# Performance work log

Hardware: AMD Instinct MI355X
Metric: run time of the kernel (lower is better)

The kernel has to match this reference:

```python
import jax, jax.numpy as jnp
import numpy as np

B = 4096
N_DENSE = 13
N_SPARSE = 26
FEAT_PER_SPARSE = 1000
FIELD_NUM = N_DENSE + N_SPARSE          # 39
FEATURE_NUM = N_DENSE + N_SPARSE * FEAT_PER_SPARSE  # 26013
K = 16


def setup_inputs() -> dict:
    key = jax.random.key(0)
    k1, k2, k3, k4 = jax.random.split(key, 4)
    dense_inputs = jax.random.normal(k1, (B, N_DENSE), dtype=jnp.float32)
    sparse_inputs = jax.random.randint(k2, (B, N_SPARSE), 0, FEAT_PER_SPARSE, dtype=jnp.int32)
    w0 = jnp.zeros((1,), dtype=jnp.float32)
    w = jax.random.normal(k3, (FEATURE_NUM, 1), dtype=jnp.float32) * 0.05
    v = jax.random.normal(k4, (FEATURE_NUM, FIELD_NUM, K), dtype=jnp.float32) * 0.05
    return {"dense_inputs": dense_inputs, "sparse_inputs": sparse_inputs,
            "w0": w0, "w": w, "v": v}


def reference(dense_inputs, sparse_inputs, w0, w, v):
    # Feature-index layout matches tf.concat([dense cols, one_hot(sparse_0), ...]):
    # rows [0, N_DENSE) of w/v belong to dense fields, then FEAT_PER_SPARSE rows per sparse field.
    offsets = N_DENSE + FEAT_PER_SPARSE * jnp.arange(N_SPARSE, dtype=sparse_inputs.dtype)
    idx = sparse_inputs + offsets[None, :]               # [B, n_sparse] global feature ids

    # First order: w0 + onehot_concat @ w  ==  w0 + dense part + gathered sparse rows
    first_order = (w0
                   + dense_inputs @ w[:N_DENSE]                       # [B, 1]
                   + jnp.sum(w[idx, 0], axis=1, keepdims=True))       # [B, 1]

    # field_f = tensordot(onehot_concat, v) -> [B, field_num, k]
    field_f = (jnp.einsum('bd,dfk->bfk', dense_inputs, v[:N_DENSE])
               + jnp.sum(v[idx], axis=1))                             # [B, F, K]

    # sum_{i<j} <f_i, f_j> = 0.5 * (||sum_i f_i||^2 - sum_i ||f_i||^2)  (FM identity)
    s = jnp.sum(field_f, axis=1)                                      # [B, K]
    second_order = 0.5 * (jnp.sum(s * s, axis=-1)
                          - jnp.sum(field_f * field_f, axis=(1, 2)))  # [B]
    return first_order + second_order[:, None]
```

## Files before the change

### kernel.cpp

```cpp
#include <hip/hip_runtime.h>

#define NDENSE 13
#define NSPARSE 26
#define ROW_F4 156
#define BATCH 4096
#define RPB 64
#define CHUNKS (BATCH / RPB)
#define SL_PER_XCD 5

__global__ __launch_bounds__(256) void ffm_slice3(
    const float*  __restrict__ dense,
    const int*    __restrict__ sparse,
    const float4* __restrict__ v4,
    float4*       __restrict__ ff)
{
    const int xcd   = blockIdx.x & 7;
    const int rest  = blockIdx.x >> 3;
    const int slice = xcd * SL_PER_XCD + (rest >> 6);
    const int chunk = rest & (CHUNKS - 1);

    __shared__ int    vrow_s[RPB * NSPARSE];
    __shared__ float  dsh   [RPB * NDENSE];
    __shared__ float4 vsh   [NDENSE * 4];

    if (slice >= 39) return;

    const int t = threadIdx.x;
    const int row0 = chunk * RPB;
    for (int i = t; i < RPB * NSPARSE; i += 256) {
        const int r = i / NSPARSE, j = i % NSPARSE;
        vrow_s[i] = sparse[(row0 + r) * NSPARSE + j] + NDENSE + 1000 * j;
    }
    for (int i = t; i < RPB * NDENSE; i += 256)
        dsh[i] = dense[row0 * NDENSE + i];
    if (t < NDENSE * 4)
        vsh[t] = v4[(t >> 2) * ROW_F4 + slice * 4 + (t & 3)];
    __syncthreads();

    const int lane = t & 63;
    const int wv   = t >> 6;
    const int rl   = (wv << 4) + (lane >> 2);
    const int c    = lane & 3;
    const int fb   = slice * 4 + c;

    float4 acc = make_float4(0.f, 0.f, 0.f, 0.f);
#pragma unroll
    for (int d = 0; d < NDENSE; ++d) {
        const float  wg = dsh[rl * NDENSE + d];
        const float4 vv = vsh[d * 4 + c];
        acc.x += wg * vv.x; acc.y += wg * vv.y;
        acc.z += wg * vv.z; acc.w += wg * vv.w;
    }

    float4 g[NSPARSE];
#pragma unroll
    for (int j = 0; j < NSPARSE; ++j)
        g[j] = v4[(unsigned)vrow_s[rl * NSPARSE + j] * ROW_F4 + fb];
#pragma unroll
    for (int j = 0; j < NSPARSE; ++j) {
        acc.x += g[j].x; acc.y += g[j].y; acc.z += g[j].z; acc.w += g[j].w;
    }

    ff[(unsigned)(row0 + rl) * ROW_F4 + fb] = acc;
}

__global__ __launch_bounds__(256) void ffm_final(
    const float*  __restrict__ dense,
    const int*    __restrict__ sparse,
    const float*  __restrict__ w0,
    const float*  __restrict__ w,
    const float4* __restrict__ ff,
    float*        __restrict__ out)
{
    const int wave = threadIdx.x >> 6;
    const int lane = threadIdx.x & 63;
    const int b = blockIdx.x * 4 + wave;

    float4 s = make_float4(0.f, 0.f, 0.f, 0.f);
    float  sq = 0.f;
#pragma unroll
    for (int p = 0; p < 3; ++p) {
        const int e4 = lane + 64 * p;
        if (e4 < ROW_F4) {
            const float4 acc = ff[(unsigned)b * ROW_F4 + e4];
            s.x += acc.x; s.y += acc.y; s.z += acc.z; s.w += acc.w;
            sq  += acc.x*acc.x + acc.y*acc.y + acc.z*acc.z + acc.w*acc.w;
        }
    }
#pragma unroll
    for (int m = 4; m <= 32; m <<= 1) {
        s.x += __shfl_xor(s.x, m); s.y += __shfl_xor(s.y, m);
        s.z += __shfl_xor(s.z, m); s.w += __shfl_xor(s.w, m);
    }
    float s2 = s.x*s.x + s.y*s.y + s.z*s.z + s.w*s.w;
    s2 += __shfl_xor(s2, 1);
    s2 += __shfl_xor(s2, 2);
#pragma unroll
    for (int m = 1; m <= 32; m <<= 1) sq += __shfl_xor(sq, m);

    float fo = 0.f;
    if (lane < NSPARSE) fo = w[sparse[b * NSPARSE + lane] + NDENSE + 1000 * lane];
    if (lane < NDENSE)  fo += dense[b * NDENSE + lane] * w[lane];
#pragma unroll
    for (int m = 1; m <= 32; m <<= 1) fo += __shfl_xor(fo, m);

    if (lane == 0) out[b] = w0[0] + fo + 0.5f * (s2 - sq);
}

__global__ __launch_bounds__(256) void ffm_fused(
    const float* __restrict__ dense, const int* __restrict__ sparse,
    const float* __restrict__ w0, const float* __restrict__ w,
    const float4* __restrict__ v4, float* __restrict__ out)
{
    const int wave = threadIdx.x >> 6;
    const int lane = threadIdx.x & 63;
    const int b = blockIdx.x * 4 + wave;

    float dv[NDENSE];
#pragma unroll
    for (int d = 0; d < NDENSE; ++d) dv[d] = dense[b * NDENSE + d];
    int myidx = 0;
    if (lane < NSPARSE) myidx = sparse[b * NSPARSE + lane] + NDENSE + 1000 * lane;

    float4 s = make_float4(0.f, 0.f, 0.f, 0.f);
    float  sq = 0.f;
#pragma unroll
    for (int p = 0; p < 3; ++p) {
        const int e4 = lane + 64 * p;
        if (e4 < ROW_F4) {
            float4 acc = make_float4(0.f, 0.f, 0.f, 0.f);
#pragma unroll
            for (int d = 0; d < NDENSE; ++d) {
                const float4 vv = v4[d * ROW_F4 + e4];
                acc.x += dv[d]*vv.x; acc.y += dv[d]*vv.y;
                acc.z += dv[d]*vv.z; acc.w += dv[d]*vv.w;
            }
#pragma unroll
            for (int j = 0; j < NSPARSE; ++j) {
                const int ij = __shfl(myidx, j);
                const float4 vv = v4[(size_t)ij * ROW_F4 + e4];
                acc.x += vv.x; acc.y += vv.y; acc.z += vv.z; acc.w += vv.w;
            }
            s.x += acc.x; s.y += acc.y; s.z += acc.z; s.w += acc.w;
            sq  += acc.x*acc.x + acc.y*acc.y + acc.z*acc.z + acc.w*acc.w;
        }
    }
#pragma unroll
    for (int m = 4; m <= 32; m <<= 1) {
        s.x += __shfl_xor(s.x, m); s.y += __shfl_xor(s.y, m);
        s.z += __shfl_xor(s.z, m); s.w += __shfl_xor(s.w, m);
    }
    float s2 = s.x*s.x + s.y*s.y + s.z*s.z + s.w*s.w;
    s2 += __shfl_xor(s2, 1);
    s2 += __shfl_xor(s2, 2);
#pragma unroll
    for (int m = 1; m <= 32; m <<= 1) sq += __shfl_xor(sq, m);
    float fo = 0.f;
    if (lane < NSPARSE) fo = w[myidx];
    if (lane < NDENSE)  fo += dense[b * NDENSE + lane] * w[lane];
#pragma unroll
    for (int m = 1; m <= 32; m <<= 1) fo += __shfl_xor(fo, m);
    if (lane == 0) out[b] = w0[0] + fo + 0.5f * (s2 - sq);
}

extern "C" void kernel_launch(void* const* d_in, const int* in_sizes, int n_in,
                              void* d_out, int out_size, void* d_ws, size_t ws_size,
                              hipStream_t stream) {
    const float*  dense  = (const float*)d_in[0];
    const int*    sparse = (const int*)d_in[1];
    const float*  w0     = (const float*)d_in[2];
    const float*  w      = (const float*)d_in[3];
    const float4* v4     = (const float4*)d_in[4];
    float* out = (float*)d_out;

    const size_t ff_bytes = (size_t)BATCH * ROW_F4 * sizeof(float4);

    if (ws_size >= ff_bytes) {
        float4* ffp = (float4*)d_ws;
        hipLaunchKernelGGL(ffm_slice3, dim3(8 * SL_PER_XCD * CHUNKS), dim3(256), 0, stream,
                           dense, sparse, v4, ffp);
        hipLaunchKernelGGL(ffm_final, dim3(BATCH / 4), dim3(256), 0, stream,
                           dense, sparse, w0, w, ffp, out);
    } else {
        hipLaunchKernelGGL(ffm_fused, dim3(BATCH / 4), dim3(256), 0, stream,
                           dense, sparse, w0, w, v4, out);
    }
}
```

Before: 39.80 us.

## Widen gather slices to 8 float4 per row with custom XCD work mapping

The slice kernel now has each row group gather 8 float4s (128 bytes) of every embedding row instead of 4, with 32 rows per block. A tail of narrow 4-wide blocks covers the last 4 float4s of the 156-float4 row. Blocks are remapped so each XCD gets a contiguous range of slice/chunk pairs, which is meant to keep the shared v rows in that XCD's L2. The sparse indices are also preloaded into registers and a sched_barrier is placed after the gathers so all loads issue before the accumulation. The aim is wider, more coalesced gathers per row and better L2 locality, at the cost of more complex indexing and a load-imbalanced tail.

```diff
diff --git a/kernel.cpp b/kernel.cpp
--- a/kernel.cpp
+++ b/kernel.cpp
@@ -4,58 +4,79 @@
 #define NSPARSE 26
 #define ROW_F4 156
 #define BATCH 4096
-#define RPB 64
-#define CHUNKS (BATCH / RPB)
-#define SL_PER_XCD 5
-
-__global__ __launch_bounds__(256) void ffm_slice3(
+
+
+__global__ __launch_bounds__(256) void ffm_slice4(
     const float*  __restrict__ dense,
     const int*    __restrict__ sparse,
     const float4* __restrict__ v4,
     float4*       __restrict__ ff)
 {
-    const int xcd   = blockIdx.x & 7;
-    const int rest  = blockIdx.x >> 3;
-    const int slice = xcd * SL_PER_XCD + (rest >> 6);
-    const int chunk = rest & (CHUNKS - 1);
-
-    __shared__ int    vrow_s[RPB * NSPARSE];
-    __shared__ float  dsh   [RPB * NDENSE];
-    __shared__ float4 vsh   [NDENSE * 4];
-
-    if (slice >= 39) return;
+    const int x = blockIdx.x & 7;
+    const int i = blockIdx.x >> 3;
+
+    bool narrow = false;
+    int fid = 0, chunk, W, sb, rpb;
+    if (x < 7) {
+        if (i >= 308) return;
+        fid = 308 * x + i;
+    } else {
+        if (i >= 340) return;
+        if (i < 276) fid = 2156 + i;
+        else { narrow = true; chunk = i - 276; }
+    }
+    if (!narrow) {
+        const int slice = fid >> 7;
+        chunk = fid & 127;
+        W = 8; sb = slice * 8; rpb = 32;
+    } else {
+        W = 4; sb = 152; rpb = 64;
+    }
+    const int row0 = chunk * rpb;
+
+    __shared__ int    vrow_s[64 * NSPARSE];
+    __shared__ float  dsh   [64 * NDENSE];
+    __shared__ float4 vsh   [NDENSE * 8];
 
     const int t = threadIdx.x;
-    const int row0 = chunk * RPB;
-    for (int i = t; i < RPB * NSPARSE; i += 256) {
-        const int r = i / NSPARSE, j = i % NSPARSE;
-        vrow_s[i] = sparse[(row0 + r) * NSPARSE + j] + NDENSE + 1000 * j;
-    }
-    for (int i = t; i < RPB * NDENSE; i += 256)
-        dsh[i] = dense[row0 * NDENSE + i];
-    if (t < NDENSE * 4)
-        vsh[t] = v4[(t >> 2) * ROW_F4 + slice * 4 + (t & 3)];
+    for (int q = t; q < rpb * NSPARSE; q += 256) {
+        const int r = q / NSPARSE, j = q % NSPARSE;
+        vrow_s[q] = sparse[(row0 + r) * NSPARSE + j] + NDENSE + 1000 * j;
+    }
+    for (int q = t; q < rpb * NDENSE; q += 256)
+        dsh[q] = dense[row0 * NDENSE + q];
+    for (int q = t; q < NDENSE * W; q += 256)
+        vsh[q] = v4[(q / W) * ROW_F4 + sb + (q % W)];
     __syncthreads();
 
     const int lane = t & 63;
     const int wv   = t >> 6;
-    const int rl   = (wv << 4) + (lane >> 2);
-    const int c    = lane & 3;
-    const int fb   = slice * 4 + c;
+    int group, c;
+    if (!narrow) { group = lane >> 3; c = lane & 7; }
+    else         { group = lane >> 2; c = lane & 3; }
+    const int rl = wv * (rpb >> 2) + group;
+    const int fb = sb + c;
 
     float4 acc = make_float4(0.f, 0.f, 0.f, 0.f);
 #pragma unroll
     for (int d = 0; d < NDENSE; ++d) {
         const float  wg = dsh[rl * NDENSE + d];
-        const float4 vv = vsh[d * 4 + c];
+        const float4 vv = vsh[d * W + c];
         acc.x += wg * vv.x; acc.y += wg * vv.y;
         acc.z += wg * vv.z; acc.w += wg * vv.w;
     }
 
+    int vrr[NSPARSE];
+#pragma unroll
+    for (int j = 0; j < NSPARSE; ++j) vrr[j] = vrow_s[rl * NSPARSE + j];
+
     float4 g[NSPARSE];
 #pragma unroll
     for (int j = 0; j < NSPARSE; ++j)
-        g[j] = v4[(unsigned)vrow_s[rl * NSPARSE + j] * ROW_F4 + fb];
+        g[j] = v4[(unsigned)vrr[j] * ROW_F4 + fb];
+
+    __builtin_amdgcn_sched_barrier(0);
+
 #pragma unroll
     for (int j = 0; j < NSPARSE; ++j) {
         acc.x += g[j].x; acc.y += g[j].y; acc.z += g[j].z; acc.w += g[j].w;
@@ -177,7 +198,7 @@
 
     if (ws_size >= ff_bytes) {
         float4* ffp = (float4*)d_ws;
-        hipLaunchKernelGGL(ffm_slice3, dim3(8 * SL_PER_XCD * CHUNKS), dim3(256), 0, stream,
+        hipLaunchKernelGGL(ffm_slice4, dim3(8 * 340), dim3(256), 0, stream,
                            dense, sparse, v4, ffp);
         hipLaunchKernelGGL(ffm_final, dim3(BATCH / 4), dim3(256), 0, stream,
                            dense, sparse, w0, w, ffp, out);
```

Result: no change. 40.54 us (+1.8%).

## Gather FP16 copy of embedding table and fuse per-slice reductions

Applied to the files above, without the earlier changes.

Adds a pre-pass that converts the whole v table to fp16 on every call, with rows padded to 80 uint4 segments. The gather kernel then reads half-width rows, with 64 columns per slice and 32 batch rows per block. It reduces each slice's partial sums and squared norms in-kernel, writing a compact partial buffer instead of the full field_f tensor. Halving gather bytes and shrinking the intermediate is meant to cut memory traffic, but the full-table conversion adds a large read and write each call, and fp16 rounding adds error. The old fused fallback for a small workspace is removed.

```diff
diff --git a/kernel.cpp b/kernel.cpp
--- a/kernel.cpp
+++ b/kernel.cpp
@@ -1,90 +1,218 @@
 #include <hip/hip_runtime.h>
+#include <hip/hip_fp16.h>
 
 #define NDENSE 13
 #define NSPARSE 26
 #define ROW_F4 156
 #define BATCH 4096
-#define RPB 64
-#define CHUNKS (BATCH / RPB)
-#define SL_PER_XCD 5
-
-__global__ __launch_bounds__(256) void ffm_slice3(
-    const float*  __restrict__ dense,
-    const int*    __restrict__ sparse,
-    const float4* __restrict__ v4,
-    float4*       __restrict__ ff)
-{
-    const int xcd   = blockIdx.x & 7;
-    const int rest  = blockIdx.x >> 3;
-    const int slice = xcd * SL_PER_XCD + (rest >> 6);
-    const int chunk = rest & (CHUNKS - 1);
-
-    __shared__ int    vrow_s[RPB * NSPARSE];
-    __shared__ float  dsh   [RPB * NDENSE];
-    __shared__ float4 vsh   [NDENSE * 4];
-
-    if (slice >= 39) return;
+#define VROWS 26013
+#define ROW_U4H 80
+#define NSLICE 10
+#define RPB 32
+#define PCHUNK 128
+#define PSTRIDE 20
+
+__global__ __launch_bounds__(256) void conv_f16(
+    const float* __restrict__ v, uint4* __restrict__ vh)
+{
+    const unsigned t = blockIdx.x * 256 + threadIdx.x;
+    if (t >= (unsigned)VROWS * ROW_U4H) return;
+    const unsigned row = t / ROW_U4H, seg = t % ROW_U4H;
+    union { __half2 h2[4]; uint4 u; } o;
+    if (seg < 78) {
+        const float4* src = (const float4*)(v + (size_t)row * 624 + seg * 8);
+        const float4 a = src[0], b = src[1];
+        o.h2[0] = __floats2half2_rn(a.x, a.y);
+        o.h2[1] = __floats2half2_rn(a.z, a.w);
+        o.h2[2] = __floats2half2_rn(b.x, b.y);
+        o.h2[3] = __floats2half2_rn(b.z, b.w);
+    } else {
+        o.u = make_uint4(0u, 0u, 0u, 0u);
+    }
+    vh[t] = o.u;
+}
+
+__global__ __launch_bounds__(256) void ffm_slice5(
+    const float* __restrict__ dense,
+    const int*   __restrict__ sparse,
+    const float* __restrict__ v,
+    const uint4* __restrict__ vh,
+    float*       __restrict__ part)
+{
+    const int x = blockIdx.x & 7;
+    const int i = blockIdx.x >> 3;
+    const int fid = x * 160 + i;
+    const int s0 = fid >> 7;
+    const int chunk = fid & (PCHUNK - 1);
+    const int row0 = chunk * RPB;
+
+    __shared__ int   vrow_s[RPB * NSPARSE];
+    __shared__ float dsh   [RPB * NDENSE];
+    __shared__ float vsh   [NDENSE * 64];
 
     const int t = threadIdx.x;
-    const int row0 = chunk * RPB;
-    for (int i = t; i < RPB * NSPARSE; i += 256) {
-        const int r = i / NSPARSE, j = i % NSPARSE;
-        vrow_s[i] = sparse[(row0 + r) * NSPARSE + j] + NDENSE + 1000 * j;
-    }
-    for (int i = t; i < RPB * NDENSE; i += 256)
-        dsh[i] = dense[row0 * NDENSE + i];
-    if (t < NDENSE * 4)
-        vsh[t] = v4[(t >> 2) * ROW_F4 + slice * 4 + (t & 3)];
+    for (int q = t; q < RPB * NSPARSE; q += 256) {
+        const int r = q / NSPARSE, j = q % NSPARSE;
+        vrow_s[q] = sparse[(row0 + r) * NSPARSE + j] + NDENSE + 1000 * j;
+    }
+    for (int q = t; q < RPB * NDENSE; q += 256)
+        dsh[q] = dense[row0 * NDENSE + q];
+    for (int q = t; q < NDENSE * 64; q += 256) {
+        const int d = q >> 6, h = q & 63, col = s0 * 64 + h;
+        vsh[q] = (col < 624) ? v[(size_t)d * 624 + col] : 0.f;
+    }
     __syncthreads();
 
     const int lane = t & 63;
     const int wv   = t >> 6;
-    const int rl   = (wv << 4) + (lane >> 2);
-    const int c    = lane & 3;
-    const int fb   = slice * 4 + c;
-
-    float4 acc = make_float4(0.f, 0.f, 0.f, 0.f);
+    const int rl   = wv * 8 + (lane >> 3);
+    const int c    = lane & 7;
+    const int rg   = row0 + rl;
+
+    float acc[8];
+#pragma unroll
+    for (int q = 0; q < 8; ++q) acc[q] = 0.f;
+
 #pragma unroll
     for (int d = 0; d < NDENSE; ++d) {
-        const float  wg = dsh[rl * NDENSE + d];
-        const float4 vv = vsh[d * 4 + c];
-        acc.x += wg * vv.x; acc.y += wg * vv.y;
-        acc.z += wg * vv.z; acc.w += wg * vv.w;
-    }
-
-    float4 g[NSPARSE];
-#pragma unroll
-    for (int j = 0; j < NSPARSE; ++j)
-        g[j] = v4[(unsigned)vrow_s[rl * NSPARSE + j] * ROW_F4 + fb];
+        const float wg = dsh[rl * NDENSE + d];
+#pragma unroll
+        for (int q = 0; q < 8; ++q)
+            acc[q] += wg * vsh[d * 64 + c * 8 + q];
+    }
+
 #pragma unroll
     for (int j = 0; j < NSPARSE; ++j) {
-        acc.x += g[j].x; acc.y += g[j].y; acc.z += g[j].z; acc.w += g[j].w;
-    }
-
-    ff[(unsigned)(row0 + rl) * ROW_F4 + fb] = acc;
-}
-
-__global__ __launch_bounds__(256) void ffm_final(
-    const float*  __restrict__ dense,
-    const int*    __restrict__ sparse,
-    const float*  __restrict__ w0,
-    const float*  __restrict__ w,
-    const float4* __restrict__ ff,
-    float*        __restrict__ out)
+        const unsigned vr = (unsigned)vrow_s[rl * NSPARSE + j];
+        union { uint4 u; __half2 h2[4]; } g;
+        g.u = vh[(size_t)vr * ROW_U4H + s0 * 8 + c];
+#pragma unroll
+        for (int q = 0; q < 4; ++q) {
+            const float2 f = __half22float2(g.h2[q]);
+            acc[2 * q]     += f.x;
+            acc[2 * q + 1] += f.y;
+        }
+    }
+
+    float sq = 0.f;
+#pragma unroll
+    for (int q = 0; q < 8; ++q) sq += acc[q] * acc[q];
+    sq += __shfl_xor(sq, 1);
+    sq += __shfl_xor(sq, 2);
+    sq += __shfl_xor(sq, 4);
+
+#pragma unroll
+    for (int q = 0; q < 8; ++q) acc[q] += __shfl_xor(acc[q], 2);
+#pragma unroll
+    for (int q = 0; q < 8; ++q) acc[q] += __shfl_xor(acc[q], 4);
+
+    float* rec = part + ((size_t)s0 * BATCH + rg) * PSTRIDE;
+    if (c < 2) {
+        float4* p = (float4*)(rec + c * 8);
+        p[0] = make_float4(acc[0], acc[1], acc[2], acc[3]);
+        p[1] = make_float4(acc[4], acc[5], acc[6], acc[7]);
+    }
+    if (c == 2) rec[16] = sq;
+}
+
+__global__ __launch_bounds__(256) void ffm_final5(
+    const float* __restrict__ dense,
+    const int*   __restrict__ sparse,
+    const float* __restrict__ w0,
+    const float* __restrict__ w,
+    const float* __restrict__ part,
+    float*       __restrict__ out)
 {
     const int wave = threadIdx.x >> 6;
     const int lane = threadIdx.x & 63;
     const int b = blockIdx.x * 4 + wave;
 
+    float sk = 0.f, sqs = 0.f;
+#pragma unroll
+    for (int s = 0; s < NSLICE; ++s) {
+        const float* rec = part + ((size_t)s * BATCH + b) * PSTRIDE;
+        if (lane < 16) sk  += rec[lane];
+        if (lane == 0) sqs += rec[16];
+    }
+    float s2 = sk * sk;
+#pragma unroll
+    for (int m = 1; m <= 32; m <<= 1) s2 += __shfl_xor(s2, m);
+
+    float fo = 0.f;
+    if (lane < NSPARSE) fo = w[sparse[b * NSPARSE + lane] + NDENSE + 1000 * lane];
+    if (lane < NDENSE)  fo += dense[b * NDENSE + lane] * w[lane];
+#pragma unroll
+    for (int m = 1; m <= 32; m <<= 1) fo += __shfl_xor(fo, m);
+
+    if (lane == 0) out[b] = w0[0] + fo + 0.5f * (s2 - sqs);
+}
+
+__global__ __launch_bounds__(256) void ffm_slice3(
+    const float* __restrict__ dense, const int* __restrict__ sparse,
+    const float4* __restrict__ v4, float4* __restrict__ ff)
+{
+    const int xcd = blockIdx.x & 7;
+    const int rest = blockIdx.x >> 3;
+    const int slice = xcd * 5 + (rest >> 6);
+    const int chunk = rest & 63;
+
+    __shared__ int    vrow_s[64 * NSPARSE];
+    __shared__ float  dshf  [64 * NDENSE];
+    __shared__ float4 vshf  [NDENSE * 4];
+
+    if (slice >= 39) return;
+    const int t = threadIdx.x;
+    const int row0 = chunk * 64;
+    for (int q = t; q < 64 * NSPARSE; q += 256) {
+        const int r = q / NSPARSE, j = q % NSPARSE;
+        vrow_s[q] = sparse[(row0 + r) * NSPARSE + j] + NDENSE + 1000 * j;
+    }
+    for (int q = t; q < 64 * NDENSE; q += 256)
+        dshf[q] = dense[row0 * NDENSE + q];
+    if (t < NDENSE * 4)
+        vshf[t] = v4[(t >> 2) * ROW_F4 + slice * 4 + (t & 3)];
+    __syncthreads();
+
+    const int lane = t & 63;
+    const int wv = t >> 6;
+    const int rl = (wv << 4) + (lane >> 2);
+    const int c = lane & 3;
+    const int fb = slice * 4 + c;
+
+    float4 acc = make_float4(0.f, 0.f, 0.f, 0.f);
+#pragma unroll
+    for (int d = 0; d < NDENSE; ++d) {
+        const float wg = dshf[rl * NDENSE + d];
+        const float4 vv = vshf[d * 4 + c];
+        acc.x += wg * vv.x; acc.y += wg * vv.y;
+        acc.z += wg * vv.z; acc.w += wg * vv.w;
+    }
+#pragma unroll
+    for (int j = 0; j < NSPARSE; ++j) {
+        const float4 g = v4[(unsigned)vrow_s[rl * NSPARSE + j] * ROW_F4 + fb];
+        acc.x += g.x; acc.y += g.y; acc.z += g.z; acc.w += g.w;
+    }
+    ff[(unsigned)(row0 + rl) * ROW_F4 + fb] = acc;
+}
+
+__global__ __launch_bounds__(256) void ffm_final(
+    const float* __restrict__ dense, const int* __restrict__ sparse,
+    const float* __restrict__ w0, const float* __restrict__ w,
+    const float4* __restrict__ ff, float* __restrict__ out)
+{
+    const int wave = threadIdx.x >> 6;
+    const int lane = threadIdx.x & 63;
+    const int b = blockIdx.x * 4 + wave;
+
     float4 s = make_float4(0.f, 0.f, 0.f, 0.f);
-    float  sq = 0.f;
+    float sq = 0.f;
 #pragma unroll
     for (int p = 0; p < 3; ++p) {
         const int e4 = lane + 64 * p;
         if (e4 < ROW_F4) {
-            const float4 acc = ff[(unsigned)b * ROW_F4 + e4];
-            s.x += acc.x; s.y += acc.y; s.z += acc.z; s.w += acc.w;
-            sq  += acc.x*acc.x + acc.y*acc.y + acc.z*acc.z + acc.w*acc.w;
+            const float4 a = ff[(unsigned)b * ROW_F4 + e4];
+            s.x += a.x; s.y += a.y; s.z += a.z; s.w += a.w;
+            sq += a.x*a.x + a.y*a.y + a.z*a.z + a.w*a.w;
         }
     }
 #pragma unroll
@@ -97,66 +225,8 @@
     s2 += __shfl_xor(s2, 2);
 #pragma unroll
     for (int m = 1; m <= 32; m <<= 1) sq += __shfl_xor(sq, m);
-
     float fo = 0.f;
     if (lane < NSPARSE) fo = w[sparse[b * NSPARSE + lane] + NDENSE + 1000 * lane];
-    if (lane < NDENSE)  fo += dense[b * NDENSE + lane] * w[lane];
-#pragma unroll
-    for (int m = 1; m <= 32; m <<= 1) fo += __shfl_xor(fo, m);
-
-    if (lane == 0) out[b] = w0[0] + fo + 0.5f * (s2 - sq);
-}
-
-__global__ __launch_bounds__(256) void ffm_fused(
-    const float* __restrict__ dense, const int* __restrict__ sparse,
-    const float* __restrict__ w0, const float* __restrict__ w,
-    const float4* __restrict__ v4, float* __restrict__ out)
-{
-    const int wave = threadIdx.x >> 6;
-    const int lane = threadIdx.x & 63;
-    const int b = blockIdx.x * 4 + wave;
-
-    float dv[NDENSE];
-#pragma unroll
-    for (int d = 0; d < NDENSE; ++d) dv[d] = dense[b * NDENSE + d];
-    int myidx = 0;
-    if (lane < NSPARSE) myidx = sparse[b * NSPARSE + lane] + NDENSE + 1000 * lane;
-
-    float4 s = make_float4(0.f, 0.f, 0.f, 0.f);
-    float  sq = 0.f;
-#pragma unroll
-    for (int p = 0; p < 3; ++p) {
-        const int e4 = lane + 64 * p;
-        if (e4 < ROW_F4) {
-            float4 acc = make_float4(0.f, 0.f, 0.f, 0.f);
-#pragma unroll
-            for (int d = 0; d < NDENSE; ++d) {
-                const float4 vv = v4[d * ROW_F4 + e4];
-                acc.x += dv[d]*vv.x; acc.y += dv[d]*vv.y;
-                acc.z += dv[d]*vv.z; acc.w += dv[d]*vv.w;
-            }
-#pragma unroll
-            for (int j = 0; j < NSPARSE; ++j) {
-                const int ij = __shfl(myidx, j);
-                const float4 vv = v4[(size_t)ij * ROW_F4 + e4];
-                acc.x += vv.x; acc.y += vv.y; acc.z += vv.z; acc.w += vv.w;
-            }
-            s.x += acc.x; s.y += acc.y; s.z += acc.z; s.w += acc.w;
-            sq  += acc.x*acc.x + acc.y*acc.y + acc.z*acc.z + acc.w*acc.w;
-        }
-    }
-#pragma unroll
-    for (int m = 4; m <= 32; m <<= 1) {
-        s.x += __shfl_xor(s.x, m); s.y += __shfl_xor(s.y, m);
-        s.z += __shfl_xor(s.z, m); s.w += __shfl_xor(s.w, m);
-    }
-    float s2 = s.x*s.x + s.y*s.y + s.z*s.z + s.w*s.w;
-    s2 += __shfl_xor(s2, 1);
-    s2 += __shfl_xor(s2, 2);
-#pragma unroll
-    for (int m = 1; m <= 32; m <<= 1) sq += __shfl_xor(sq, m);
-    float fo = 0.f;
-    if (lane < NSPARSE) fo = w[myidx];
     if (lane < NDENSE)  fo += dense[b * NDENSE + lane] * w[lane];
 #pragma unroll
     for (int m = 1; m <= 32; m <<= 1) fo += __shfl_xor(fo, m);
@@ -170,19 +240,29 @@
     const int*    sparse = (const int*)d_in[1];
     const float*  w0     = (const float*)d_in[2];
     const float*  w      = (const float*)d_in[3];
+    const float*  v      = (const float*)d_in[4];
     const float4* v4     = (const float4*)d_in[4];
     float* out = (float*)d_out;
 
-    const size_t ff_bytes = (size_t)BATCH * ROW_F4 * sizeof(float4);
-
-    if (ws_size >= ff_bytes) {
+    const size_t vh_bytes   = (size_t)VROWS * ROW_U4H * 16;
+    const size_t part_bytes = (size_t)NSLICE * BATCH * PSTRIDE * 4;
+    const size_t ff_bytes   = (size_t)BATCH * ROW_F4 * sizeof(float4);
+
+    if (ws_size >= vh_bytes + part_bytes) {
+        uint4* vh   = (uint4*)d_ws;
+        float* prt  = (float*)((char*)d_ws + vh_bytes);
+        const unsigned convN = (unsigned)VROWS * ROW_U4H;
+        hipLaunchKernelGGL(conv_f16, dim3((convN + 255) / 256), dim3(256), 0, stream,
+                           v, vh);
+        hipLaunchKernelGGL(ffm_slice5, dim3(8 * 160), dim3(256), 0, stream,
+                           dense, sparse, v, vh, prt);
+        hipLaunchKernelGGL(ffm_final5, dim3(BATCH / 4), dim3(256), 0, stream,
+                           dense, sparse, w0, w, prt, out);
+    } else if (ws_size >= ff_bytes) {
         float4* ffp = (float4*)d_ws;
-        hipLaunchKernelGGL(ffm_slice3, dim3(8 * SL_PER_XCD * CHUNKS), dim3(256), 0, stream,
+        hipLaunchKernelGGL(ffm_slice3, dim3(8 * 5 * 64), dim3(256), 0, stream,
                            dense, sparse, v4, ffp);
         hipLaunchKernelGGL(ffm_final, dim3(BATCH / 4), dim3(256), 0, stream,
                            dense, sparse, w0, w, ffp, out);
-    } else {
-        hipLaunchKernelGGL(ffm_fused, dim3(BATCH / 4), dim3(256), 0, stream,
-                           dense, sparse, w0, w, v4, out);
-    }
-}
+    }
+}
```

Result: no change. 40.19 us (+1.0%).
